# Optimization experiments

Hardware: AMD Instinct MI355X
Metric: run time of the kernel (lower is better)

Reference implementation:

```python
import jax, jax.numpy as jnp
import numpy as np

B, S, D, E, F, K = 2, 4096, 1024, 8, 2048, 2


def setup_inputs() -> dict:
    key = jax.random.key(0)
    k1, k2, k3, k4 = jax.random.split(key, 4)
    return {
        "inputs_raw": jax.random.normal(k1, (B, S, D), dtype=jnp.float32),
        "gate_w": jax.random.normal(k2, (D, E), dtype=jnp.float32) * (D ** -0.5),
        "w1": jax.random.normal(k3, (E, D, F), dtype=jnp.float32) * (D ** -0.5),
        "w2": jax.random.normal(k4, (E, F, D), dtype=jnp.float32) * (F ** -0.5),
        "top_k": K,
    }


def reference(inputs_raw, gate_w, w1, w2, top_k):
    ishape = inputs_raw.shape
    x = inputs_raw.reshape(-1, ishape[-1])                 # [T, D]
    n_experts = gate_w.shape[-1]

    # --- gating: top-k logits, softmax over the selected k (float32, like the torch code) ---
    logits = x @ gate_w                                    # [T, E]
    top_vals, top_idx = jax.lax.top_k(logits, top_k)       # [T, K]
    top_w = jax.nn.softmax(top_vals.astype(jnp.float32), axis=-1).astype(x.dtype)
    # dense combine weights [T, E]; zero for unselected experts
    combine = jnp.einsum("tk,tke->te", top_w,
                         jax.nn.one_hot(top_idx, n_experts, dtype=x.dtype))

    # --- experts: D -> F (SiLU) -> D, evaluated densely and combined with gate weights ---
    h = jax.nn.silu(jnp.einsum("td,edf->etf", x, w1))      # [E, T, F]
    y = jnp.einsum("etf,efd->etd", h, w2)                  # [E, T, D]
    out = jnp.einsum("te,etd->td", combine, y)             # [T, D]
    return out.reshape(ishape)
```

## Files before the change

kernel.cpp:

```cpp
#include <hip/hip_runtime.h>
#include <cstdint>
#include <cstddef>

#define T_TOK 8192
#define DIM   1024
#define NE    8
#define FF    2048
#define TOPK  2

typedef __bf16 bf16x8 __attribute__((ext_vector_type(8)));
typedef float  floatx4 __attribute__((ext_vector_type(4)));

__device__ __forceinline__ unsigned short f2bf(float f) {
  unsigned int u = __float_as_uint(f);
  unsigned int r = 0x7FFFu + ((u >> 16) & 1u);
  return (unsigned short)((u + r) >> 16);
}

__device__ __forceinline__ void gl_lds16(const void* g, void* l) {
  __builtin_amdgcn_global_load_lds(
      (__attribute__((address_space(1))) void*)g,
      (__attribute__((address_space(3))) void*)l,
      16, 0, 0);
}

__global__ __launch_bounds__(256) void transpose2_bf16_kernel(
    const float* __restrict__ w1, unsigned short* __restrict__ w1t,
    const float* __restrict__ w2, unsigned short* __restrict__ w2t)
{
  __shared__ float tile[32][33];
  int z = blockIdx.z;
  int e = z & 7, sel = z >> 3;
  int R = sel ? FF : DIM;
  int C = sel ? DIM : FF;
  const float* inp = (sel ? w2 : w1) + (size_t)e * R * C;
  unsigned short* op = (sel ? w2t : w1t) + (size_t)e * R * C;
  int nc = C >> 5;
  int bx = blockIdx.x;
  int c0 = (bx % nc) * 32, r0 = (bx / nc) * 32;
  int tx = threadIdx.x & 31, ty = threadIdx.x >> 5;
  for (int i = 0; i < 4; ++i)
    tile[ty + i * 8][tx] = inp[(size_t)(r0 + ty + i * 8) * C + c0 + tx];
  __syncthreads();
  for (int i = 0; i < 4; ++i)
    op[(size_t)(c0 + ty + i * 8) * R + r0 + tx] = f2bf(tile[tx][ty + i * 8]);
}

__global__ __launch_bounds__(256) void gate_kernel(
    const float* __restrict__ x, const float* __restrict__ gw,
    unsigned short* __restrict__ xb, int* __restrict__ tokExp,
    float* __restrict__ tokW, int* __restrict__ cnt)
{
  __shared__ float gwT[NE][DIM];
  int tid = threadIdx.x;
  if (blockIdx.x == 0 && tid < NE) cnt[tid] = 0;
  for (int i = tid; i < DIM * NE; i += 256) {
    int d = i >> 3, e = i & 7;
    gwT[e][d] = gw[i];
  }
  __syncthreads();

  int wv = tid >> 6, lane = tid & 63;
  int t = blockIdx.x * 4 + wv;
  const float* xrow = x + (size_t)t * DIM;
  unsigned short* xbrow = xb + (size_t)t * DIM;

  double acc[NE];
  for (int e = 0; e < NE; ++e) acc[e] = 0.0;

  for (int j = 0; j < 4; ++j) {
    float4 xv = ((const float4*)xrow)[j * 64 + lane];
    ushort4 s;
    s.x = f2bf(xv.x); s.y = f2bf(xv.y); s.z = f2bf(xv.z); s.w = f2bf(xv.w);
    ((ushort4*)xbrow)[j * 64 + lane] = s;
    double xd0 = (double)xv.x, xd1 = (double)xv.y;
    double xd2 = (double)xv.z, xd3 = (double)xv.w;
    for (int e = 0; e < NE; ++e) {
      float4 g = ((const float4*)&gwT[e][0])[j * 64 + lane];
      acc[e] += xd0 * (double)g.x + xd1 * (double)g.y +
                xd2 * (double)g.z + xd3 * (double)g.w;
    }
  }

  for (int s = 32; s > 0; s >>= 1)
    for (int e = 0; e < NE; ++e)
      acc[e] += __shfl_down(acc[e], s, 64);

  if (lane == 0) {
    int e0 = 0; double v0 = acc[0];
    for (int e = 1; e < NE; ++e) if (acc[e] > v0) { v0 = acc[e]; e0 = e; }
    int e1 = -1; double v1 = -1.0e300;
    for (int e = 0; e < NE; ++e) {
      if (e == e0) continue;
      if (acc[e] > v1) { v1 = acc[e]; e1 = e; }
    }
    float a = (float)v0, b = (float)v1;
    float eb = __expf(b - a);
    float den = 1.0f + eb;
    tokExp[t] = e0 | (e1 << 8);
    tokW[2 * t + 0] = 1.0f / den;
    tokW[2 * t + 1] = eb / den;
  }
}

__global__ __launch_bounds__(256) void assign_kernel(
    const int* __restrict__ tokExp, int* __restrict__ tokEnc,
    int* __restrict__ tIdx, int* __restrict__ cnt)
{
  int t = blockIdx.x * 256 + threadIdx.x;
  int lane = threadIdx.x & 63;
  unsigned long long below = (1ull << lane) - 1ull;
  int enc = tokExp[t];
  int e0 = enc & 0xFF, e1 = (enc >> 8) & 0xFF;
  int s0 = 0, s1 = 0;
  for (int e = 0; e < NE; ++e) {
    unsigned long long m0 = __ballot(e0 == e);
    unsigned long long m1 = __ballot(e1 == e);
    int c0 = __popcll(m0), c1 = __popcll(m1);
    int base = 0;
    if (lane == 0 && (c0 + c1) > 0)
      base = atomicAdd(&cnt[e], c0 + c1);
    base = __shfl(base, 0, 64);
    if (e0 == e) s0 = base + __popcll(m0 & below);
    if (e1 == e) s1 = base + c0 + __popcll(m1 & below);
  }
  tokEnc[2 * t + 0] = (e0 << 16) | s0;
  tokEnc[2 * t + 1] = (e1 << 16) | s1;
  tIdx[e0 * T_TOK + s0] = t;
  tIdx[e1 * T_TOK + s1] = t;
}

__global__ __launch_bounds__(256, 4) void gemm1_kernel(
    const unsigned short* __restrict__ xb,
    const unsigned short* __restrict__ w1t,
    unsigned short* __restrict__ h,
    const int* __restrict__ tIdx, const int* __restrict__ cnt)
{
  int g = blockIdx.x;
  int e = g & 7;
  int b = g >> 3;
  int phase = b >> 9;
  int m = (b >> 3) & 63;
  int nl = b & 7;
  int count = cnt[e];
  int r0 = m * 128;
  if (r0 >= count) return;
  int n0 = (phase * 8 + nl) * 128;

  __shared__ __align__(16) unsigned short As[8][128][8];
  __shared__ __align__(16) unsigned short Bs[8][128][8];

  int tid = threadIdx.x, lane = tid & 63, w = tid >> 6;
  int wr = w >> 1, wc = w & 1;
  int quad = lane >> 4, li = lane & 15;

  const unsigned short* ag[2];
  const unsigned short* bg[2];
  for (int c = 0; c < 2; ++c) {
    int mm = c * 64 + lane;
    int r = r0 + mm; if (r > count - 1) r = count - 1;
    ag[c] = xb + (size_t)tIdx[e * T_TOK + r] * DIM;
    bg[c] = w1t + ((size_t)e * FF + (n0 + mm)) * DIM;
  }

  floatx4 acc[4][4];
  for (int mi = 0; mi < 4; ++mi)
    for (int ni = 0; ni < 4; ++ni)
      for (int q = 0; q < 4; ++q) acc[mi][ni][q] = 0.0f;

  for (int k0 = 0; k0 < DIM; k0 += 64) {
    __syncthreads();
    for (int kk = 0; kk < 2; ++kk) {
      int kq = w + kk * 4;
      gl_lds16(ag[0] + k0 + kq * 8, &As[kq][0][0]);
      gl_lds16(ag[1] + k0 + kq * 8, &As[kq][64][0]);
      gl_lds16(bg[0] + k0 + kq * 8, &Bs[kq][0][0]);
      gl_lds16(bg[1] + k0 + kq * 8, &Bs[kq][64][0]);
    }
    __syncthreads();
    for (int ks = 0; ks < 2; ++ks) {
      bf16x8 af[4], bf[4];
      for (int mi = 0; mi < 4; ++mi)
        af[mi] = *(const bf16x8*)&As[ks * 4 + quad][wr * 64 + mi * 16 + li][0];
      for (int ni = 0; ni < 4; ++ni)
        bf[ni] = *(const bf16x8*)&Bs[ks * 4 + quad][wc * 64 + ni * 16 + li][0];
      for (int mi = 0; mi < 4; ++mi)
        for (int ni = 0; ni < 4; ++ni)
          acc[mi][ni] = __builtin_amdgcn_mfma_f32_16x16x32_bf16(
              af[mi], bf[ni], acc[mi][ni], 0, 0, 0);
    }
  }

  size_t hb = 0;
  for (int i = 0; i < e; ++i) hb += cnt[i];
  for (int mi = 0; mi < 4; ++mi) {
    int rowb = wr * 64 + mi * 16 + quad * 4;
    for (int rr = 0; rr < 4; ++rr) {
      int r = r0 + rowb + rr;
      if (r >= count) continue;
      unsigned short* hrow = h + (hb + r) * FF + n0 + wc * 64 + li;
      for (int ni = 0; ni < 4; ++ni) {
        float v = acc[mi][ni][rr];
        float s = v / (1.0f + __expf(-v));
        hrow[ni * 16] = f2bf(s);
      }
    }
  }
}

__global__ __launch_bounds__(256, 4) void gemm2_kernel(
    const unsigned short* __restrict__ h,
    const unsigned short* __restrict__ w2t,
    float* __restrict__ yv,
    const int* __restrict__ cnt)
{
  int g = blockIdx.x;
  int e = g & 7;
  int b = g >> 3;
  int phase = b >> 8;
  int m = (b >> 2) & 63;
  int nl = b & 3;
  int count = cnt[e];
  int r0 = m * 128;
  if (r0 >= count) return;
  int n0 = (phase * 4 + nl) * 128;

  __shared__ __align__(16) unsigned short As[8][128][8];
  __shared__ __align__(16) unsigned short Bs[8][128][8];

  int tid = threadIdx.x, lane = tid & 63, w = tid >> 6;
  int wr = w >> 1, wc = w & 1;
  int quad = lane >> 4, li = lane & 15;
  size_t yb = 0;
  for (int i = 0; i < e; ++i) yb += cnt[i];

  const unsigned short* ag[2];
  const unsigned short* bg[2];
  for (int c = 0; c < 2; ++c) {
    int mm = c * 64 + lane;
    int r = r0 + mm; if (r > count - 1) r = count - 1;
    ag[c] = h + (yb + r) * FF;
    bg[c] = w2t + ((size_t)e * DIM + (n0 + mm)) * FF;
  }

  floatx4 acc[4][4];
  for (int mi = 0; mi < 4; ++mi)
    for (int ni = 0; ni < 4; ++ni)
      for (int q = 0; q < 4; ++q) acc[mi][ni][q] = 0.0f;

  for (int k0 = 0; k0 < FF; k0 += 64) {
    __syncthreads();
    for (int kk = 0; kk < 2; ++kk) {
      int kq = w + kk * 4;
      gl_lds16(ag[0] + k0 + kq * 8, &As[kq][0][0]);
      gl_lds16(ag[1] + k0 + kq * 8, &As[kq][64][0]);
      gl_lds16(bg[0] + k0 + kq * 8, &Bs[kq][0][0]);
      gl_lds16(bg[1] + k0 + kq * 8, &Bs[kq][64][0]);
    }
    __syncthreads();
    for (int ks = 0; ks < 2; ++ks) {
      bf16x8 af[4], bf[4];
      for (int mi = 0; mi < 4; ++mi)
        af[mi] = *(const bf16x8*)&As[ks * 4 + quad][wr * 64 + mi * 16 + li][0];
      for (int ni = 0; ni < 4; ++ni)
        bf[ni] = *(const bf16x8*)&Bs[ks * 4 + quad][wc * 64 + ni * 16 + li][0];
      for (int mi = 0; mi < 4; ++mi)
        for (int ni = 0; ni < 4; ++ni)
          acc[mi][ni] = __builtin_amdgcn_mfma_f32_16x16x32_bf16(
              af[mi], bf[ni], acc[mi][ni], 0, 0, 0);
    }
  }

  for (int mi = 0; mi < 4; ++mi) {
    int rowb = wr * 64 + mi * 16 + quad * 4;
    for (int rr = 0; rr < 4; ++rr) {
      int r = r0 + rowb + rr;
      if (r >= count) continue;
      float* yrow = yv + (yb + r) * DIM + n0 + wc * 64 + li;
      for (int ni = 0; ni < 4; ++ni)
        yrow[ni * 16] = acc[mi][ni][rr];
    }
  }
}

__global__ __launch_bounds__(256) void combine_kernel(
    const float* __restrict__ yv, const int* __restrict__ tokEnc,
    const float* __restrict__ tokW, const int* __restrict__ cnt,
    float* __restrict__ out)
{
  int t = blockIdx.x;
  int i = threadIdx.x;
  int enc0 = tokEnc[2 * t + 0], enc1 = tokEnc[2 * t + 1];
  float w0 = tokW[2 * t + 0], w1 = tokW[2 * t + 1];
  int x0 = enc0 >> 16, x1 = enc1 >> 16;
  int off0 = 0, off1 = 0, a = 0;
  for (int e = 0; e < NE; ++e) {
    if (e == x0) off0 = a;
    if (e == x1) off1 = a;
    a += cnt[e];
  }
  size_t row0 = (size_t)off0 + (enc0 & 0xFFFF);
  size_t row1 = (size_t)off1 + (enc1 & 0xFFFF);
  float4 va = ((const float4*)(yv + row0 * DIM))[i];
  float4 vb = ((const float4*)(yv + row1 * DIM))[i];
  float4 o;
  o.x = w0 * va.x + w1 * vb.x;
  o.y = w0 * va.y + w1 * vb.y;
  o.z = w0 * va.z + w1 * vb.z;
  o.w = w0 * va.w + w1 * vb.w;
  ((float4*)(out + (size_t)t * DIM))[i] = o;
}

extern "C" void kernel_launch(void* const* d_in, const int* in_sizes, int n_in,
                              void* d_out, int out_size, void* d_ws, size_t ws_size,
                              hipStream_t stream)
{
  const float* x  = (const float*)d_in[0];
  const float* gw = (const float*)d_in[1];
  const float* w1 = (const float*)d_in[2];
  const float* w2 = (const float*)d_in[3];
  float* out = (float*)d_out;

  size_t o = 0;
  auto alloc = [&](size_t bytes) {
    void* p = (char*)d_ws + o;
    o += (bytes + 255) & ~(size_t)255;
    return p;
  };
  unsigned short* xb   = (unsigned short*)alloc((size_t)T_TOK * DIM * 2);
  unsigned short* w1t  = (unsigned short*)alloc((size_t)NE * DIM * FF * 2);
  unsigned short* w2t  = (unsigned short*)alloc((size_t)NE * DIM * FF * 2);
  unsigned short* hbuf = (unsigned short*)alloc((size_t)T_TOK * TOPK * FF * 2);
  float*          yv   = (float*)alloc((size_t)T_TOK * TOPK * DIM * 4);
  int*   tIdx   = (int*)alloc((size_t)NE * T_TOK * 4);
  int*   tokEnc = (int*)alloc((size_t)2 * T_TOK * 4);
  float* tokW   = (float*)alloc((size_t)2 * T_TOK * 4);
  int*   tokExp = (int*)alloc((size_t)T_TOK * 4);
  int*   cnt    = (int*)alloc((size_t)NE * 4);

  transpose2_bf16_kernel<<<dim3(2048, 1, 2 * NE), 256, 0, stream>>>(w1, w1t, w2, w2t);

  gate_kernel<<<T_TOK / 4, 256, 0, stream>>>(x, gw, xb, tokExp, tokW, cnt);
  assign_kernel<<<T_TOK / 256, 256, 0, stream>>>(tokExp, tokEnc, tIdx, cnt);

  gemm1_kernel<<<8192, 256, 0, stream>>>(xb, w1t, hbuf, tIdx, cnt);
  gemm2_kernel<<<4096, 256, 0, stream>>>(hbuf, w2t, yv, cnt);
  combine_kernel<<<T_TOK, 256, 0, stream>>>(yv, tokEnc, tokW, cnt, out);
}
```

Before: 544.7 us.

## Fuse combine into gemm2 via weighted atomic scatter; widen weight transpose tiles

Removes the intermediate yv buffer and the separate combine kernel. gemm2 now scales each output row by its gate weight and atomically adds it into the output token row, and gate_kernel zeroes the output beforehand. The assign step now stores a per-slot gate weight array instead of token encodings. Separately, the weight transpose uses 64x64 tiles with float4 loads, converts to bf16 before staging in LDS, and writes ushort4 vectors. The atomics add contention and make the order of the two-expert fp32 sum nondeterministic.

```diff
diff --git a/kernel.cpp b/kernel.cpp
--- a/kernel.cpp
+++ b/kernel.cpp
@@ -28,32 +28,53 @@
     const float* __restrict__ w1, unsigned short* __restrict__ w1t,
     const float* __restrict__ w2, unsigned short* __restrict__ w2t)
 {
-  __shared__ float tile[32][33];
+  __shared__ unsigned short tile[64][68];
   int z = blockIdx.z;
   int e = z & 7, sel = z >> 3;
   int R = sel ? FF : DIM;
   int C = sel ? DIM : FF;
   const float* inp = (sel ? w2 : w1) + (size_t)e * R * C;
   unsigned short* op = (sel ? w2t : w1t) + (size_t)e * R * C;
-  int nc = C >> 5;
+  int nc = C >> 6;
   int bx = blockIdx.x;
-  int c0 = (bx % nc) * 32, r0 = (bx / nc) * 32;
-  int tx = threadIdx.x & 31, ty = threadIdx.x >> 5;
-  for (int i = 0; i < 4; ++i)
-    tile[ty + i * 8][tx] = inp[(size_t)(r0 + ty + i * 8) * C + c0 + tx];
+  int c0 = (bx % nc) * 64, r0 = (bx / nc) * 64;
+  int t4 = threadIdx.x & 15, ry = threadIdx.x >> 4;
+  #pragma unroll
+  for (int p = 0; p < 4; ++p) {
+    int r = ry + p * 16;
+    float4 v = *(const float4*)&inp[(size_t)(r0 + r) * C + c0 + t4 * 4];
+    ushort4 sv;
+    sv.x = f2bf(v.x); sv.y = f2bf(v.y); sv.z = f2bf(v.z); sv.w = f2bf(v.w);
+    *(ushort4*)&tile[r][t4 * 4] = sv;
+  }
   __syncthreads();
-  for (int i = 0; i < 4; ++i)
-    op[(size_t)(c0 + ty + i * 8) * R + r0 + tx] = f2bf(tile[tx][ty + i * 8]);
+  #pragma unroll
+  for (int p = 0; p < 4; ++p) {
+    int cy = ry + p * 16;
+    ushort4 s;
+    s.x = tile[t4 * 4 + 0][cy];
+    s.y = tile[t4 * 4 + 1][cy];
+    s.z = tile[t4 * 4 + 2][cy];
+    s.w = tile[t4 * 4 + 3][cy];
+    *(ushort4*)&op[(size_t)(c0 + cy) * R + r0 + t4 * 4] = s;
+  }
 }
 
 __global__ __launch_bounds__(256) void gate_kernel(
     const float* __restrict__ x, const float* __restrict__ gw,
     unsigned short* __restrict__ xb, int* __restrict__ tokExp,
-    float* __restrict__ tokW, int* __restrict__ cnt)
+    float* __restrict__ tokW, int* __restrict__ cnt,
+    float* __restrict__ out)
 {
   __shared__ float gwT[NE][DIM];
   int tid = threadIdx.x;
   if (blockIdx.x == 0 && tid < NE) cnt[tid] = 0;
+  {
+    float4 z4 = make_float4(0.f, 0.f, 0.f, 0.f);
+    float4* ob = (float4*)out + (size_t)blockIdx.x * 1024;
+    #pragma unroll
+    for (int i = 0; i < 4; ++i) ob[i * 256 + tid] = z4;
+  }
   for (int i = tid; i < DIM * NE; i += 256) {
     int d = i >> 3, e = i & 7;
     gwT[e][d] = gw[i];
@@ -104,8 +125,8 @@
 }
 
 __global__ __launch_bounds__(256) void assign_kernel(
-    const int* __restrict__ tokExp, int* __restrict__ tokEnc,
-    int* __restrict__ tIdx, int* __restrict__ cnt)
+    const int* __restrict__ tokExp, const float* __restrict__ tokW,
+    int* __restrict__ tIdx, float* __restrict__ tokW2, int* __restrict__ cnt)
 {
   int t = blockIdx.x * 256 + threadIdx.x;
   int lane = threadIdx.x & 63;
@@ -124,10 +145,10 @@
     if (e0 == e) s0 = base + __popcll(m0 & below);
     if (e1 == e) s1 = base + c0 + __popcll(m1 & below);
   }
-  tokEnc[2 * t + 0] = (e0 << 16) | s0;
-  tokEnc[2 * t + 1] = (e1 << 16) | s1;
   tIdx[e0 * T_TOK + s0] = t;
   tIdx[e1 * T_TOK + s1] = t;
+  tokW2[e0 * T_TOK + s0] = tokW[2 * t + 0];
+  tokW2[e1 * T_TOK + s1] = tokW[2 * t + 1];
 }
 
 __global__ __launch_bounds__(256, 4) void gemm1_kernel(
@@ -211,7 +232,8 @@
 __global__ __launch_bounds__(256, 4) void gemm2_kernel(
     const unsigned short* __restrict__ h,
     const unsigned short* __restrict__ w2t,
-    float* __restrict__ yv,
+    float* out,
+    const int* __restrict__ tIdx, const float* __restrict__ tokW2,
     const int* __restrict__ cnt)
 {
   int g = blockIdx.x;
@@ -276,39 +298,13 @@
     for (int rr = 0; rr < 4; ++rr) {
       int r = r0 + rowb + rr;
       if (r >= count) continue;
-      float* yrow = yv + (yb + r) * DIM + n0 + wc * 64 + li;
+      int t = tIdx[e * T_TOK + r];
+      float wgt = tokW2[e * T_TOK + r];
+      float* orow = out + (size_t)t * DIM + n0 + wc * 64 + li;
       for (int ni = 0; ni < 4; ++ni)
-        yrow[ni * 16] = acc[mi][ni][rr];
-    }
-  }
-}
-
-__global__ __launch_bounds__(256) void combine_kernel(
-    const float* __restrict__ yv, const int* __restrict__ tokEnc,
-    const float* __restrict__ tokW, const int* __restrict__ cnt,
-    float* __restrict__ out)
-{
-  int t = blockIdx.x;
-  int i = threadIdx.x;
-  int enc0 = tokEnc[2 * t + 0], enc1 = tokEnc[2 * t + 1];
-  float w0 = tokW[2 * t + 0], w1 = tokW[2 * t + 1];
-  int x0 = enc0 >> 16, x1 = enc1 >> 16;
-  int off0 = 0, off1 = 0, a = 0;
-  for (int e = 0; e < NE; ++e) {
-    if (e == x0) off0 = a;
-    if (e == x1) off1 = a;
-    a += cnt[e];
-  }
-  size_t row0 = (size_t)off0 + (enc0 & 0xFFFF);
-  size_t row1 = (size_t)off1 + (enc1 & 0xFFFF);
-  float4 va = ((const float4*)(yv + row0 * DIM))[i];
-  float4 vb = ((const float4*)(yv + row1 * DIM))[i];
-  float4 o;
-  o.x = w0 * va.x + w1 * vb.x;
-  o.y = w0 * va.y + w1 * vb.y;
-  o.z = w0 * va.z + w1 * vb.z;
-  o.w = w0 * va.w + w1 * vb.w;
-  ((float4*)(out + (size_t)t * DIM))[i] = o;
+        atomicAdd(&orow[ni * 16], wgt * acc[mi][ni][rr]);
+    }
+  }
 }
 
 extern "C" void kernel_launch(void* const* d_in, const int* in_sizes, int n_in,
@@ -331,19 +327,17 @@
   unsigned short* w1t  = (unsigned short*)alloc((size_t)NE * DIM * FF * 2);
   unsigned short* w2t  = (unsigned short*)alloc((size_t)NE * DIM * FF * 2);
   unsigned short* hbuf = (unsigned short*)alloc((size_t)T_TOK * TOPK * FF * 2);
-  float*          yv   = (float*)alloc((size_t)T_TOK * TOPK * DIM * 4);
   int*   tIdx   = (int*)alloc((size_t)NE * T_TOK * 4);
-  int*   tokEnc = (int*)alloc((size_t)2 * T_TOK * 4);
+  float* tokW2  = (float*)alloc((size_t)NE * T_TOK * 4);
   float* tokW   = (float*)alloc((size_t)2 * T_TOK * 4);
   int*   tokExp = (int*)alloc((size_t)T_TOK * 4);
   int*   cnt    = (int*)alloc((size_t)NE * 4);
 
-  transpose2_bf16_kernel<<<dim3(2048, 1, 2 * NE), 256, 0, stream>>>(w1, w1t, w2, w2t);
-
-  gate_kernel<<<T_TOK / 4, 256, 0, stream>>>(x, gw, xb, tokExp, tokW, cnt);
-  assign_kernel<<<T_TOK / 256, 256, 0, stream>>>(tokExp, tokEnc, tIdx, cnt);
+  transpose2_bf16_kernel<<<dim3(512, 1, 2 * NE), 256, 0, stream>>>(w1, w1t, w2, w2t);
+
+  gate_kernel<<<T_TOK / 4, 256, 0, stream>>>(x, gw, xb, tokExp, tokW, cnt, out);
+  assign_kernel<<<T_TOK / 256, 256, 0, stream>>>(tokExp, tokW, tIdx, tokW2, cnt);
 
   gemm1_kernel<<<8192, 256, 0, stream>>>(xb, w1t, hbuf, tIdx, cnt);
-  gemm2_kernel<<<4096, 256, 0, stream>>>(hbuf, w2t, yv, cnt);
-  combine_kernel<<<T_TOK, 256, 0, stream>>>(yv, tokEnc, tokW, cnt, out);
-}
+  gemm2_kernel<<<4096, 256, 0, stream>>>(hbuf, w2t, out, tIdx, tokW2, cnt);
+}
```

Result: no change. 551.7 us (+1.3%).

## Fuse weight transpose and gating into one prep kernel with 64x64 vectorized tiles

Applied to the files above, without the earlier changes.

Merges the weight transpose/bf16 conversion kernel and the gating kernel into a single launch, so the extra blocks do the transpose while the first blocks do gating. The transpose now uses 64x64 tiles with float4 loads, converts to bf16 before storing into shared memory, and writes ushort4 vectors, cutting the number of memory transactions. The aim is to remove a launch and serialization between the two kernels and raise transpose bandwidth. In exchange, the bf16 shared tile with stride 68 may see bank conflicts on the column reads, and both paths now share one shared memory allocation.

```diff
diff --git a/kernel.cpp b/kernel.cpp
--- a/kernel.cpp
+++ b/kernel.cpp
@@ -24,36 +24,54 @@
       16, 0, 0);
 }
 
-__global__ __launch_bounds__(256) void transpose2_bf16_kernel(
+__global__ __launch_bounds__(256) void prep_kernel(
     const float* __restrict__ w1, unsigned short* __restrict__ w1t,
-    const float* __restrict__ w2, unsigned short* __restrict__ w2t)
-{
-  __shared__ float tile[32][33];
-  int z = blockIdx.z;
-  int e = z & 7, sel = z >> 3;
-  int R = sel ? FF : DIM;
-  int C = sel ? DIM : FF;
-  const float* inp = (sel ? w2 : w1) + (size_t)e * R * C;
-  unsigned short* op = (sel ? w2t : w1t) + (size_t)e * R * C;
-  int nc = C >> 5;
-  int bx = blockIdx.x;
-  int c0 = (bx % nc) * 32, r0 = (bx / nc) * 32;
-  int tx = threadIdx.x & 31, ty = threadIdx.x >> 5;
-  for (int i = 0; i < 4; ++i)
-    tile[ty + i * 8][tx] = inp[(size_t)(r0 + ty + i * 8) * C + c0 + tx];
-  __syncthreads();
-  for (int i = 0; i < 4; ++i)
-    op[(size_t)(c0 + ty + i * 8) * R + r0 + tx] = f2bf(tile[tx][ty + i * 8]);
-}
-
-__global__ __launch_bounds__(256) void gate_kernel(
+    const float* __restrict__ w2, unsigned short* __restrict__ w2t,
     const float* __restrict__ x, const float* __restrict__ gw,
     unsigned short* __restrict__ xb, int* __restrict__ tokExp,
     float* __restrict__ tokW, int* __restrict__ cnt)
 {
-  __shared__ float gwT[NE][DIM];
+  __shared__ __align__(16) char smem[NE * DIM * 4];
   int tid = threadIdx.x;
-  if (blockIdx.x == 0 && tid < NE) cnt[tid] = 0;
+  int b = blockIdx.x;
+
+  if (b >= T_TOK / 4) {
+    unsigned short (*tile)[68] = (unsigned short (*)[68])smem;
+    int t64 = b - T_TOK / 4;
+    int z = t64 >> 9;
+    int e = z & 7, sel = z >> 3;
+    int R = sel ? FF : DIM;
+    int C = sel ? DIM : FF;
+    const float* inp = (sel ? w2 : w1) + (size_t)e * R * C;
+    unsigned short* op = (sel ? w2t : w1t) + (size_t)e * R * C;
+    int nc = C >> 6;
+    int bx = t64 & 511;
+    int c0 = (bx % nc) * 64, r0 = (bx / nc) * 64;
+    int t4 = tid & 15, ry = tid >> 4;
+    #pragma unroll
+    for (int p = 0; p < 4; ++p) {
+      int r = ry + p * 16;
+      float4 v = *(const float4*)&inp[(size_t)(r0 + r) * C + c0 + t4 * 4];
+      ushort4 sv;
+      sv.x = f2bf(v.x); sv.y = f2bf(v.y); sv.z = f2bf(v.z); sv.w = f2bf(v.w);
+      *(ushort4*)&tile[r][t4 * 4] = sv;
+    }
+    __syncthreads();
+    #pragma unroll
+    for (int p = 0; p < 4; ++p) {
+      int cy = ry + p * 16;
+      ushort4 s;
+      s.x = tile[t4 * 4 + 0][cy];
+      s.y = tile[t4 * 4 + 1][cy];
+      s.z = tile[t4 * 4 + 2][cy];
+      s.w = tile[t4 * 4 + 3][cy];
+      *(ushort4*)&op[(size_t)(c0 + cy) * R + r0 + t4 * 4] = s;
+    }
+    return;
+  }
+
+  float (*gwT)[DIM] = (float (*)[DIM])smem;
+  if (b == 0 && tid < NE) cnt[tid] = 0;
   for (int i = tid; i < DIM * NE; i += 256) {
     int d = i >> 3, e = i & 7;
     gwT[e][d] = gw[i];
@@ -61,7 +79,7 @@
   __syncthreads();
 
   int wv = tid >> 6, lane = tid & 63;
-  int t = blockIdx.x * 4 + wv;
+  int t = b * 4 + wv;
   const float* xrow = x + (size_t)t * DIM;
   unsigned short* xbrow = xb + (size_t)t * DIM;
 
@@ -94,8 +112,8 @@
       if (e == e0) continue;
       if (acc[e] > v1) { v1 = acc[e]; e1 = e; }
     }
-    float a = (float)v0, b = (float)v1;
-    float eb = __expf(b - a);
+    float a = (float)v0, bb = (float)v1;
+    float eb = __expf(bb - a);
     float den = 1.0f + eb;
     tokExp[t] = e0 | (e1 << 8);
     tokW[2 * t + 0] = 1.0f / den;
@@ -338,9 +356,9 @@
   int*   tokExp = (int*)alloc((size_t)T_TOK * 4);
   int*   cnt    = (int*)alloc((size_t)NE * 4);
 
-  transpose2_bf16_kernel<<<dim3(2048, 1, 2 * NE), 256, 0, stream>>>(w1, w1t, w2, w2t);
-
-  gate_kernel<<<T_TOK / 4, 256, 0, stream>>>(x, gw, xb, tokExp, tokW, cnt);
+  prep_kernel<<<T_TOK / 4 + 8192, 256, 0, stream>>>(
+      w1, w1t, w2, w2t, x, gw, xb, tokExp, tokW, cnt);
+
   assign_kernel<<<T_TOK / 256, 256, 0, stream>>>(tokExp, tokEnc, tIdx, cnt);
 
   gemm1_kernel<<<8192, 256, 0, stream>>>(xb, w1t, hbuf, tIdx, cnt);
```

Result: no change. 538.1 us (-1.2%).
